# Optimization experiments

Measured on AMD Instinct MI355X. Metric: run time of the kernel, lower is better.

Reference implementation:

```python
import jax, jax.numpy as jnp
import numpy as np

NUM_ITERS = 10
G_KSIZE, G_SIGMA = 5, 0.5
BIL_KSIZE, BIL_SIG_COLOR, BIL_SIG_SPACE = 5, 0.5, 5.0
EDGE_KSIZE, EDGE_SIG_COLOR, EDGE_SIG_SPACE = 5, 0.5, 5.0


def _gauss1d(ksize, sigma):
    x = jnp.arange(ksize, dtype=jnp.float32) - ksize // 2  # odd ksize -> centered (kornia)
    g = jnp.exp(-(x * x) / (2.0 * sigma * sigma))
    return g / g.sum()


def gaussian_blur(q, ksize, sigma):
    # separable gaussian blur with reflect padding, kornia GaussianBlur2d semantics
    k = _gauss1d(ksize, sigma)
    r = ksize // 2
    B, C, H, W = q.shape
    qp = jnp.pad(q, ((0, 0), (0, 0), (r, r), (0, 0)), mode='reflect')
    q = sum(k[i] * qp[:, :, i:i + H, :] for i in range(ksize))
    qp = jnp.pad(q, ((0, 0), (0, 0), (0, 0), (r, r)), mode='reflect')
    q = sum(k[i] * qp[:, :, :, i:i + W] for i in range(ksize))
    return q


def bilateral_weights(guide, ksize, sigma_color, sigma_space):
    # kornia joint_bilateral_blur weights (l1 color distance, reflect border).
    # guide: [B, Cg, H, W] -> weights [B, K*K, H, W]; guidance is constant across
    # CRF iterations so we precompute the kernel once.
    B, Cg, H, W = guide.shape
    r = ksize // 2
    g1 = _gauss1d(ksize, sigma_space)
    space = jnp.outer(g1, g1)  # normalized 2d gaussian (kornia get_gaussian_kernel2d)
    gp = jnp.pad(guide, ((0, 0), (0, 0), (r, r), (r, r)), mode='reflect')
    inv2sc2 = -0.5 / (sigma_color * sigma_color)
    ws = []
    for dy in range(ksize):
        for dx in range(ksize):
            d = jnp.abs(gp[:, :, dy:dy + H, dx:dx + W] - guide).sum(axis=1)  # [B,H,W]
            ws.append(space[dy, dx] * jnp.exp(inv2sc2 * d * d))
    return jnp.stack(ws, axis=1)  # [B, K*K, H, W]


def bilateral_apply(q, weights, ksize):
    # q: [B,C,H,W], weights: [B,K*K,H,W]
    B, C, H, W = q.shape
    r = ksize // 2
    qp = jnp.pad(q, ((0, 0), (0, 0), (r, r), (r, r)), mode='reflect')
    num = jnp.zeros_like(q)
    idx = 0
    for dy in range(ksize):
        for dx in range(ksize):
            num = num + weights[:, idx][:, None] * qp[:, :, dy:dy + H, dx:dx + W]
            idx += 1
    den = weights.sum(axis=1)[:, None]  # [B,1,H,W]
    return num / den


def _compat(f):
    # compat matrix is -1 off-diagonal, 0 on diagonal:
    # pairwise[c] = -sum_{c'!=c} f[c'] = f[c] - sum_{c'} f[c']
    return f - f.sum(axis=1, keepdims=True)


def setup_inputs() -> dict:
    key = jax.random.key(0)
    k1, k2, k3 = jax.random.split(key, 3)
    B, C, H, W = 2, 21, 512, 512
    unary_logits = jax.random.normal(k1, (B, C, H, W), dtype=jnp.float32)
    image = jax.random.uniform(k2, (B, 3, H, W), dtype=jnp.float32)
    edges = jax.random.uniform(k3, (B, H, W), dtype=jnp.float32)
    return {"unary_logits": unary_logits, "image": image, "edges": edges}


def reference(unary_logits, image, edges):
    edges4 = edges[:, None]  # [B,1,H,W]
    w_rgb = bilateral_weights(image, BIL_KSIZE, BIL_SIG_COLOR, BIL_SIG_SPACE)
    w_edge = bilateral_weights(edges4, EDGE_KSIZE, EDGE_SIG_COLOR, EDGE_SIG_SPACE)
    q = jax.nn.softmax(unary_logits, axis=1)
    for _ in range(NUM_ITERS):
        sf = gaussian_blur(q, G_KSIZE, G_SIGMA)
        rf = bilateral_apply(q, w_rgb, BIL_KSIZE)
        ef = bilateral_apply(q, w_edge, EDGE_KSIZE)
        pairwise = _compat(sf) + _compat(rf) + _compat(ef)
        q = jax.nn.softmax(unary_logits - pairwise, axis=1)
    return q
```

## Files before the change

### kernel.cpp

```cpp
#include <hip/hip_runtime.h>
#include <math.h>

#define BATCH 2
#define NCH 21
#define CPAD 24
#define HH 512
#define WW 512
#define KS 5
#define RAD 2
#define NTAPS 25
#define NUM_ITERS 10

#define TXW 32
#define TYW 8
#define HXW (TXW + 2*RAD)
#define HYW (TYW + 2*RAD)
#define HPXW (HXW * HYW)

#define TW 32
#define TH 16
#define NTHR 512
#define SX 40
#define SY 24
#define SPX (SX * SY)
#define SCHUNK (SPX * 3)
#define EX 36
#define EY 20
#define EPX (EX * EY)
#define RING (EPX - TW*TH)

typedef _Float16 f16;
typedef _Float16 half8 __attribute__((ext_vector_type(8)));
typedef _Float16 half2v __attribute__((ext_vector_type(2)));

__device__ __forceinline__ int refl(int i, int n) {
    if (i < 0) i = -i;
    if (i >= n) i = 2*n - 2 - i;
    return i;
}

#define WSEL(h0, h1, h2, hl, t) \
    ((t) < 8 ? (h0)[(t)] : (t) < 16 ? (h1)[(t) - 8] : (t) < 24 ? (h2)[(t) - 16] : (hl))

__global__ __launch_bounds__(256) void weights_kernel(const float* __restrict__ image,
                                                      const float* __restrict__ edges,
                                                      f16* __restrict__ wcA,
                                                      f16* __restrict__ wcB16) {
    __shared__ float sr_[HYW][HXW];
    __shared__ float sg_[HYW][HXW];
    __shared__ float sb_[HYW][HXW];
    __shared__ float se_[HYW][HXW];

    const int tx = threadIdx.x;
    const int ty = threadIdx.y;
    const int tid = ty * TXW + tx;
    const int x0 = blockIdx.x * TXW;
    const int y0 = blockIdx.y * TYW;
    const int b = blockIdx.z;
    const int x = x0 + tx;
    const int y = y0 + ty;
    const size_t plane = (size_t)HH * WW;
    const float* img = image + (size_t)b * 3 * plane;
    const float* edg = edges + (size_t)b * plane;

    for (int i = tid; i < HPXW; i += TXW * TYW) {
        int ly = i / HXW, lx = i - ly * HXW;
        int gy = refl(y0 + ly - RAD, HH);
        int gx = refl(x0 + lx - RAD, WW);
        int g = gy * WW + gx;
        sr_[ly][lx] = img[g];
        sg_[ly][lx] = img[plane + g];
        sb_[ly][lx] = img[2 * plane + g];
        se_[ly][lx] = edg[g];
    }
    __syncthreads();

    float gs[3];
    gs[0] = 1.0f; gs[1] = __expf(-1.0f / 50.0f); gs[2] = __expf(-4.0f / 50.0f);
    float gb[3];
    gb[0] = 1.0f; gb[1] = __expf(-2.0f); gb[2] = __expf(-8.0f);
    float gbs = gb[0] + 2.0f * (gb[1] + gb[2]);
    gb[0] /= gbs; gb[1] /= gbs; gb[2] /= gbs;

    const float r0 = sr_[ty + RAD][tx + RAD];
    const float g0 = sg_[ty + RAD][tx + RAD];
    const float b0 = sb_[ty + RAD][tx + RAD];
    const float e0 = se_[ty + RAD][tx + RAD];

    float wr[NTAPS], we[NTAPS];
    float sr = 0.f, se = 0.f;
#pragma unroll
    for (int dy = 0; dy < KS; dy++) {
#pragma unroll
        for (int dx = 0; dx < KS; dx++) {
            float sp = gs[abs(dy - RAD)] * gs[abs(dx - RAD)];
            float d = fabsf(sr_[ty + dy][tx + dx] - r0)
                    + fabsf(sg_[ty + dy][tx + dx] - g0)
                    + fabsf(sb_[ty + dy][tx + dx] - b0);
            float w1 = sp * __expf(-2.0f * d * d);
            float de = fabsf(se_[ty + dy][tx + dx] - e0);
            float w2 = sp * __expf(-2.0f * de * de);
            wr[dy * KS + dx] = w1;
            we[dy * KS + dx] = w2;
            sr += w1;
            se += w2;
        }
    }
    float isr = 1.0f / sr, ise = 1.0f / se;
    float wt[NTAPS];
#pragma unroll
    for (int t = 0; t < NTAPS; t++) {
        int dy = t / KS, dx = t % KS;
        float g2 = gb[abs(dy - RAD)] * gb[abs(dx - RAD)];
        wt[t] = g2 + wr[t] * isr + we[t] * ise;
    }
    const size_t pixoff = (size_t)b * plane + (size_t)y * WW + x;
    half8* wo = (half8*)(wcA + pixoff * 24);
#pragma unroll
    for (int g = 0; g < 3; g++) {
        half8 v;
#pragma unroll
        for (int k = 0; k < 8; k++) v[k] = (f16)wt[g * 8 + k];
        wo[g] = v;
    }
    wcB16[pixoff] = (f16)wt[24];
}

__global__ void init_kernel(const float* __restrict__ unary,
                            f16* __restrict__ q,
                            f16* __restrict__ u16) {
    int idx = blockIdx.x * blockDim.x + threadIdx.x;
    if (idx >= BATCH * HH * WW) return;
    int p = idx % (HH * WW);
    int b = idx / (HH * WW);
    const size_t plane = (size_t)HH * WW;
    const float* u = unary + (size_t)b * NCH * plane + p;
    float l[CPAD];
    float m = -1e30f;
#pragma unroll
    for (int c = 0; c < NCH; c++) { l[c] = u[c * plane]; m = fmaxf(m, l[c]); }
    l[21] = 0.f; l[22] = 0.f; l[23] = 0.f;

    half8* uo = (half8*)(u16 + ((size_t)b * plane + p) * CPAD);
#pragma unroll
    for (int g = 0; g < 3; g++) {
        half8 v;
#pragma unroll
        for (int k = 0; k < 8; k++) v[k] = (f16)l[g * 8 + k];
        uo[g] = v;
    }

    float s = 0.f;
    float e[CPAD];
#pragma unroll
    for (int c = 0; c < NCH; c++) { e[c] = __expf(l[c] - m); s += e[c]; }
    float is = 1.0f / s;
    e[21] = 0.f; e[22] = 0.f; e[23] = 0.f;
    half8* qo = (half8*)(q + ((size_t)b * plane + p) * CPAD);
#pragma unroll
    for (int g = 0; g < 3; g++) {
        half8 v;
#pragma unroll
        for (int k = 0; k < 8; k++) v[k] = (f16)(e[g * 8 + k] * is);
        qo[g] = v;
    }
}

#define CONV_ACC_PK(acc2, lds, row0, col0, stride, W0, W1, W2, WL)                     \
    {                                                                                  \
        _Pragma("unroll")                                                              \
        for (int dy = 0; dy < KS; dy++) {                                              \
            _Pragma("unroll")                                                          \
            for (int dx = 0; dx < KS; dx++) {                                          \
                const f16 wt_ = WSEL(W0, W1, W2, WL, dy * KS + dx);                    \
                const half2v wv_ = {wt_, wt_};                                         \
                const f16* tp = (lds) + ((size_t)((row0) + dy) * (stride) + (col0) + dx) * CPAD; \
                half8 v0 = *(const half8*)(tp);                                        \
                half8 v1 = *(const half8*)(tp + 8);                                    \
                half8 v2 = *(const half8*)(tp + 16);                                   \
                acc2[0]  = __builtin_elementwise_fma(wv_, __builtin_shufflevector(v0, v0, 0, 1), acc2[0]);  \
                acc2[1]  = __builtin_elementwise_fma(wv_, __builtin_shufflevector(v0, v0, 2, 3), acc2[1]);  \
                acc2[2]  = __builtin_elementwise_fma(wv_, __builtin_shufflevector(v0, v0, 4, 5), acc2[2]);  \
                acc2[3]  = __builtin_elementwise_fma(wv_, __builtin_shufflevector(v0, v0, 6, 7), acc2[3]);  \
                acc2[4]  = __builtin_elementwise_fma(wv_, __builtin_shufflevector(v1, v1, 0, 1), acc2[4]);  \
                acc2[5]  = __builtin_elementwise_fma(wv_, __builtin_shufflevector(v1, v1, 2, 3), acc2[5]);  \
                acc2[6]  = __builtin_elementwise_fma(wv_, __builtin_shufflevector(v1, v1, 4, 5), acc2[6]);  \
                acc2[7]  = __builtin_elementwise_fma(wv_, __builtin_shufflevector(v1, v1, 6, 7), acc2[7]);  \
                acc2[8]  = __builtin_elementwise_fma(wv_, __builtin_shufflevector(v2, v2, 0, 1), acc2[8]);  \
                acc2[9]  = __builtin_elementwise_fma(wv_, __builtin_shufflevector(v2, v2, 2, 3), acc2[9]);  \
                acc2[10] = __builtin_elementwise_fma(wv_, __builtin_shufflevector(v2, v2, 4, 5), acc2[10]); \
            }                                                                          \
        }                                                                              \
    }

#define LOGITS_FROM_PK(l, acc2, U0, U1, U2)                                            \
    {                                                                                  \
        _Pragma("unroll")                                                              \
        for (int j = 0; j < 10; j++) {                                                 \
            l[2 * j]     = -(float)acc2[j][0];                                         \
            l[2 * j + 1] = -(float)acc2[j][1];                                         \
        }                                                                              \
        l[20] = -(float)acc2[10][0];                                                   \
        _Pragma("unroll")                                                              \
        for (int k = 0; k < 8; k++) l[k] += (float)U0[k];                              \
        _Pragma("unroll")                                                              \
        for (int k = 0; k < 8; k++) l[8 + k] += (float)U1[k];                          \
        _Pragma("unroll")                                                              \
        for (int k = 0; k < 5; k++) l[16 + k] += (float)U2[k];                         \
    }

template <bool FINAL>
__global__ __launch_bounds__(NTHR, 4) void crf_pair_kernel(const f16* __restrict__ qin,
                                                           const f16* __restrict__ u16,
                                                           const f16* __restrict__ wcA,
                                                           const f16* __restrict__ wcB16,
                                                           void* __restrict__ qout) {
    __shared__ __align__(16) f16 buf[SPX][CPAD];

    const int tid = threadIdx.x;
    const int ix = tid & (TW - 1);
    const int iy = tid >> 5;

    const int flat = blockIdx.x;
    const int band = flat & 7;
    const int within = flat >> 3;
    const int b = within >> 6;
    const int r = within & 63;
    const int x0 = (r & 15) * TW;
    const int y0 = (band * 4 + (r >> 4)) * TH;
    const int gx = x0 + ix;
    const int gy = y0 + iy;
    const size_t plane = (size_t)HH * WW;

    const f16* qbase = qin + (size_t)b * plane * CPAD;
    f16* lbase = &buf[0][0];
    for (int idx = tid; idx < SCHUNK; idx += NTHR) {
        int px = idx / 3, h4 = idx - px * 3;
        int sly = px / SX, slx = px - sly * SX;
        int qy = refl(y0 - 4 + sly, HH);
        int qx = refl(x0 - 4 + slx, WW);
        const f16* g = qbase + ((size_t)(qy * WW + qx)) * CPAD + h4 * 8;
        __builtin_amdgcn_global_load_lds(
            (const __attribute__((address_space(1))) void*)g,
            (__attribute__((address_space(3))) void*)(lbase + (size_t)idx * 8),
            16, 0, 0);
    }

    const size_t pixoff = (size_t)b * plane + (size_t)gy * WW + gx;
    const half8* wp = (const half8*)(wcA + pixoff * 24);
    half8 wa0 = wp[0], wa1 = wp[1], wa2 = wp[2];
    f16 wl = wcB16[pixoff];
    const half8* up = (const half8*)(u16 + pixoff * CPAD);
    half8 ui0 = up[0], ui1 = up[1], ui2 = up[2];

    const bool has_ring = tid < RING;
    int rly = 0, rlx = 0;
    half8 wr0 = {}, wr1 = {}, wr2 = {}, ur0 = {}, ur1 = {}, ur2 = {};
    f16 wrl = (f16)0.f;
    if (has_ring) {
        int t = tid;
        if (t < 72)       { rly = t / 36;       rlx = t % 36; }
        else if (t < 144) { t -= 72;  rly = 18 + t / 36; rlx = t % 36; }
        else              { t -= 144; rly = 2 + (t >> 2); int c = t & 3; rlx = (c < 2) ? c : (c + 32); }
        int rgy = y0 + rly - 2, rgx = x0 + rlx - 2;
        int cy = min(max(rgy, 0), HH - 1);
        int cx = min(max(rgx, 0), WW - 1);
        size_t rpo = (size_t)b * plane + (size_t)cy * WW + cx;
        const half8* wpr = (const half8*)(wcA + rpo * 24);
        wr0 = wpr[0]; wr1 = wpr[1]; wr2 = wpr[2];
        wrl = wcB16[rpo];
        const half8* upr = (const half8*)(u16 + rpo * CPAD);
        ur0 = upr[0]; ur1 = upr[1]; ur2 = upr[2];
    }

    __syncthreads();

    half8 qr0, qr1, qr2;
    if (has_ring) {
        half2v acc2[11];
#pragma unroll
        for (int j = 0; j < 11; j++) acc2[j] = (half2v){(f16)0.f, (f16)0.f};
        CONV_ACC_PK(acc2, lbase, rly, rlx, SX, wr0, wr1, wr2, wrl);
        float l[NCH];
        LOGITS_FROM_PK(l, acc2, ur0, ur1, ur2);
        float m = l[0];
#pragma unroll
        for (int c = 1; c < NCH; c++) m = fmaxf(m, l[c]);
        float s = 0.f;
#pragma unroll
        for (int c = 0; c < NCH; c++) { l[c] = __expf(l[c] - m); s += l[c]; }
        float is = 1.0f / s;
#pragma unroll
        for (int k = 0; k < 8; k++) qr0[k] = (f16)(l[k] * is);
#pragma unroll
        for (int k = 0; k < 8; k++) qr1[k] = (f16)(l[8 + k] * is);
#pragma unroll
        for (int k = 0; k < 5; k++) qr2[k] = (f16)(l[16 + k] * is);
        qr2[5] = (f16)0.f; qr2[6] = (f16)0.f; qr2[7] = (f16)0.f;
    }

    half8 qi0, qi1, qi2;
    {
        half2v acc2[11];
#pragma unroll
        for (int j = 0; j < 11; j++) acc2[j] = (half2v){(f16)0.f, (f16)0.f};
        CONV_ACC_PK(acc2, lbase, iy + 2, ix + 2, SX, wa0, wa1, wa2, wl);
        float l[NCH];
        LOGITS_FROM_PK(l, acc2, ui0, ui1, ui2);
        float m = l[0];
#pragma unroll
        for (int c = 1; c < NCH; c++) m = fmaxf(m, l[c]);
        float s = 0.f;
#pragma unroll
        for (int c = 0; c < NCH; c++) { l[c] = __expf(l[c] - m); s += l[c]; }
        float is = 1.0f / s;
#pragma unroll
        for (int k = 0; k < 8; k++) qi0[k] = (f16)(l[k] * is);
#pragma unroll
        for (int k = 0; k < 8; k++) qi1[k] = (f16)(l[8 + k] * is);
#pragma unroll
        for (int k = 0; k < 5; k++) qi2[k] = (f16)(l[16 + k] * is);
        qi2[5] = (f16)0.f; qi2[6] = (f16)0.f; qi2[7] = (f16)0.f;
    }

    __syncthreads();

    {
        half8* d = (half8*)(lbase + ((size_t)(iy + 2) * EX + (ix + 2)) * CPAD);
        d[0] = qi0; d[1] = qi1; d[2] = qi2;
        if (has_ring) {
            half8* dr = (half8*)(lbase + ((size_t)rly * EX + rlx) * CPAD);
            dr[0] = qr0; dr[1] = qr1; dr[2] = qr2;
        }
    }

    __syncthreads();

    {
        int ry[KS], rx[KS];
#pragma unroll
        for (int d = 0; d < KS; d++) {
            ry[d] = refl(gy + d - 2, HH) - (y0 - 2);
            rx[d] = refl(gx + d - 2, WW) - (x0 - 2);
        }
        half2v acc2[11];
#pragma unroll
        for (int j = 0; j < 11; j++) acc2[j] = (half2v){(f16)0.f, (f16)0.f};
#pragma unroll
        for (int dy = 0; dy < KS; dy++) {
#pragma unroll
            for (int dx = 0; dx < KS; dx++) {
                const f16 wt_ = WSEL(wa0, wa1, wa2, wl, dy * KS + dx);
                const half2v wv_ = {wt_, wt_};
                const f16* tp = lbase + ((size_t)ry[dy] * EX + rx[dx]) * CPAD;
                half8 v0 = *(const half8*)(tp);
                half8 v1 = *(const half8*)(tp + 8);
                half8 v2 = *(const half8*)(tp + 16);
                acc2[0]  = __builtin_elementwise_fma(wv_, __builtin_shufflevector(v0, v0, 0, 1), acc2[0]);
                acc2[1]  = __builtin_elementwise_fma(wv_, __builtin_shufflevector(v0, v0, 2, 3), acc2[1]);
                acc2[2]  = __builtin_elementwise_fma(wv_, __builtin_shufflevector(v0, v0, 4, 5), acc2[2]);
                acc2[3]  = __builtin_elementwise_fma(wv_, __builtin_shufflevector(v0, v0, 6, 7), acc2[3]);
                acc2[4]  = __builtin_elementwise_fma(wv_, __builtin_shufflevector(v1, v1, 0, 1), acc2[4]);
                acc2[5]  = __builtin_elementwise_fma(wv_, __builtin_shufflevector(v1, v1, 2, 3), acc2[5]);
                acc2[6]  = __builtin_elementwise_fma(wv_, __builtin_shufflevector(v1, v1, 4, 5), acc2[6]);
                acc2[7]  = __builtin_elementwise_fma(wv_, __builtin_shufflevector(v1, v1, 6, 7), acc2[7]);
                acc2[8]  = __builtin_elementwise_fma(wv_, __builtin_shufflevector(v2, v2, 0, 1), acc2[8]);
                acc2[9]  = __builtin_elementwise_fma(wv_, __builtin_shufflevector(v2, v2, 2, 3), acc2[9]);
                acc2[10] = __builtin_elementwise_fma(wv_, __builtin_shufflevector(v2, v2, 4, 5), acc2[10]);
            }
        }
        float l[NCH];
        LOGITS_FROM_PK(l, acc2, ui0, ui1, ui2);
        float m = l[0];
#pragma unroll
        for (int c = 1; c < NCH; c++) m = fmaxf(m, l[c]);
        float s = 0.f;
#pragma unroll
        for (int c = 0; c < NCH; c++) { l[c] = __expf(l[c] - m); s += l[c]; }
        float is = 1.0f / s;

        if (FINAL) {
            float* qo = (float*)qout + (size_t)b * NCH * plane + (size_t)gy * WW + gx;
#pragma unroll
            for (int c = 0; c < NCH; c++) qo[c * plane] = l[c] * is;
        } else {
            half8* qo = (half8*)((f16*)qout + pixoff * CPAD);
            half8 o0, o1, o2;
#pragma unroll
            for (int k = 0; k < 8; k++) o0[k] = (f16)(l[k] * is);
#pragma unroll
            for (int k = 0; k < 8; k++) o1[k] = (f16)(l[8 + k] * is);
#pragma unroll
            for (int k = 0; k < 5; k++) o2[k] = (f16)(l[16 + k] * is);
            o2[5] = (f16)0.f; o2[6] = (f16)0.f; o2[7] = (f16)0.f;
            qo[0] = o0; qo[1] = o1; qo[2] = o2;
        }
    }
}

extern "C" void kernel_launch(void* const* d_in, const int* in_sizes, int n_in,
                              void* d_out, int out_size, void* d_ws, size_t ws_size,
                              hipStream_t stream) {
    const float* unary = (const float*)d_in[0];
    const float* image = (const float*)d_in[1];
    const float* edges = (const float*)d_in[2];
    float* out = (float*)d_out;

    const size_t plane = (size_t)HH * WW;
    char* ws = (char*)d_ws;
    f16* wcA = (f16*)ws;
    char* p1 = ws + sizeof(f16) * BATCH * plane * 24;
    f16* wcB16 = (f16*)p1;
    char* p2 = p1 + sizeof(f16) * BATCH * plane;
    f16* u16 = (f16*)p2;
    char* p3 = p2 + sizeof(f16) * BATCH * plane * CPAD;
    f16* qA = (f16*)p3;
    f16* qB = qA + (size_t)BATCH * plane * CPAD;

    const int npix = BATCH * HH * WW;
    dim3 gridW(WW / TXW, HH / TYW, BATCH);
    dim3 blockW(TXW, TYW, 1);
    weights_kernel<<<gridW, blockW, 0, stream>>>(image, edges, wcA, wcB16);
    init_kernel<<<(npix + 255) / 256, 256, 0, stream>>>(unary, qA, u16);

    const int nblk = (WW / TW) * (HH / TH) * BATCH;
    f16* qa = qA;
    f16* qb = qB;
    const int npairs = NUM_ITERS / 2;
    for (int it = 0; it < npairs - 1; it++) {
        crf_pair_kernel<false><<<nblk, NTHR, 0, stream>>>(qa, u16, wcA, wcB16, (void*)qb);
        f16* t = qa; qa = qb; qb = t;
    }
    crf_pair_kernel<true><<<nblk, NTHR, 0, stream>>>(qa, u16, wcA, wcB16, (void*)out);
}
```

Before: 287.4 us.

## Compute two vertically adjacent pixels per thread to share LDS loads

Halves the thread count per block and has each thread compute two vertically adjacent output pixels. The thread walks 6 staged rows and feeds each loaded LDS neighbour into both pixels' accumulators, which cuts LDS reads per pixel. The ring (halo) work is remapped so each ring thread also handles two rows. The cost is roughly double the accumulator and weight registers per thread, which may lower occupancy (launch bounds now 256 threads, 3 blocks).

```diff
diff --git a/kernel.cpp b/kernel.cpp
--- a/kernel.cpp
+++ b/kernel.cpp
@@ -19,7 +19,7 @@
 
 #define TW 32
 #define TH 16
-#define NTHR 512
+#define NTHRP 256
 #define SX 40
 #define SY 24
 #define SPX (SX * SY)
@@ -27,7 +27,7 @@
 #define EX 36
 #define EY 20
 #define EPX (EX * EY)
-#define RING (EPX - TW*TH)
+#define RINGP 104
 
 typedef _Float16 f16;
 typedef _Float16 half8 __attribute__((ext_vector_type(8)));
@@ -166,31 +166,68 @@
     }
 }
 
-#define CONV_ACC_PK(acc2, lds, row0, col0, stride, W0, W1, W2, WL)                     \
-    {                                                                                  \
-        _Pragma("unroll")                                                              \
-        for (int dy = 0; dy < KS; dy++) {                                              \
-            _Pragma("unroll")                                                          \
-            for (int dx = 0; dx < KS; dx++) {                                          \
-                const f16 wt_ = WSEL(W0, W1, W2, WL, dy * KS + dx);                    \
-                const half2v wv_ = {wt_, wt_};                                         \
-                const f16* tp = (lds) + ((size_t)((row0) + dy) * (stride) + (col0) + dx) * CPAD; \
-                half8 v0 = *(const half8*)(tp);                                        \
-                half8 v1 = *(const half8*)(tp + 8);                                    \
-                half8 v2 = *(const half8*)(tp + 16);                                   \
-                acc2[0]  = __builtin_elementwise_fma(wv_, __builtin_shufflevector(v0, v0, 0, 1), acc2[0]);  \
-                acc2[1]  = __builtin_elementwise_fma(wv_, __builtin_shufflevector(v0, v0, 2, 3), acc2[1]);  \
-                acc2[2]  = __builtin_elementwise_fma(wv_, __builtin_shufflevector(v0, v0, 4, 5), acc2[2]);  \
-                acc2[3]  = __builtin_elementwise_fma(wv_, __builtin_shufflevector(v0, v0, 6, 7), acc2[3]);  \
-                acc2[4]  = __builtin_elementwise_fma(wv_, __builtin_shufflevector(v1, v1, 0, 1), acc2[4]);  \
-                acc2[5]  = __builtin_elementwise_fma(wv_, __builtin_shufflevector(v1, v1, 2, 3), acc2[5]);  \
-                acc2[6]  = __builtin_elementwise_fma(wv_, __builtin_shufflevector(v1, v1, 4, 5), acc2[6]);  \
-                acc2[7]  = __builtin_elementwise_fma(wv_, __builtin_shufflevector(v1, v1, 6, 7), acc2[7]);  \
-                acc2[8]  = __builtin_elementwise_fma(wv_, __builtin_shufflevector(v2, v2, 0, 1), acc2[8]);  \
-                acc2[9]  = __builtin_elementwise_fma(wv_, __builtin_shufflevector(v2, v2, 2, 3), acc2[9]);  \
-                acc2[10] = __builtin_elementwise_fma(wv_, __builtin_shufflevector(v2, v2, 4, 5), acc2[10]); \
-            }                                                                          \
-        }                                                                              \
+#define PK11(acc2, wv_, v0, v1, v2) do {                                                            \
+    acc2[0]  = __builtin_elementwise_fma(wv_, __builtin_shufflevector(v0, v0, 0, 1), acc2[0]);      \
+    acc2[1]  = __builtin_elementwise_fma(wv_, __builtin_shufflevector(v0, v0, 2, 3), acc2[1]);      \
+    acc2[2]  = __builtin_elementwise_fma(wv_, __builtin_shufflevector(v0, v0, 4, 5), acc2[2]);      \
+    acc2[3]  = __builtin_elementwise_fma(wv_, __builtin_shufflevector(v0, v0, 6, 7), acc2[3]);      \
+    acc2[4]  = __builtin_elementwise_fma(wv_, __builtin_shufflevector(v1, v1, 0, 1), acc2[4]);      \
+    acc2[5]  = __builtin_elementwise_fma(wv_, __builtin_shufflevector(v1, v1, 2, 3), acc2[5]);      \
+    acc2[6]  = __builtin_elementwise_fma(wv_, __builtin_shufflevector(v1, v1, 4, 5), acc2[6]);      \
+    acc2[7]  = __builtin_elementwise_fma(wv_, __builtin_shufflevector(v1, v1, 6, 7), acc2[7]);      \
+    acc2[8]  = __builtin_elementwise_fma(wv_, __builtin_shufflevector(v2, v2, 0, 1), acc2[8]);      \
+    acc2[9]  = __builtin_elementwise_fma(wv_, __builtin_shufflevector(v2, v2, 2, 3), acc2[9]);      \
+    acc2[10] = __builtin_elementwise_fma(wv_, __builtin_shufflevector(v2, v2, 4, 5), acc2[10]);     \
+} while (0)
+
+#define CONV_PAIR_STAGED(accA, accB, lds, row0, col0, stride,                                       \
+                         WA0, WA1, WA2, WAL, WB0, WB1, WB2, WBL)                                    \
+    {                                                                                               \
+        _Pragma("unroll")                                                                           \
+        for (int r_ = 0; r_ < 6; r_++) {                                                            \
+            _Pragma("unroll")                                                                       \
+            for (int dx_ = 0; dx_ < 5; dx_++) {                                                     \
+                const f16* tp_ = (lds) + ((size_t)((row0) + r_) * (stride) + (col0) + dx_) * CPAD;  \
+                half8 v0_ = *(const half8*)(tp_);                                                   \
+                half8 v1_ = *(const half8*)(tp_ + 8);                                               \
+                half8 v2_ = *(const half8*)(tp_ + 16);                                              \
+                if (r_ < 5) {                                                                       \
+                    const f16 wA_ = WSEL(WA0, WA1, WA2, WAL, r_ * 5 + dx_);                         \
+                    const half2v wvA_ = {wA_, wA_};                                                 \
+                    PK11(accA, wvA_, v0_, v1_, v2_);                                                \
+                }                                                                                   \
+                if (r_ >= 1) {                                                                      \
+                    const f16 wB_ = WSEL(WB0, WB1, WB2, WBL, (r_ - 1) * 5 + dx_);                   \
+                    const half2v wvB_ = {wB_, wB_};                                                 \
+                    PK11(accB, wvB_, v0_, v1_, v2_);                                                \
+                }                                                                                   \
+            }                                                                                       \
+        }                                                                                           \
+    }
+
+#define CONV_PAIR_IDX(accA, accB, lds, ryArr, rxArr, stride,                                        \
+                      WA0, WA1, WA2, WAL, WB0, WB1, WB2, WBL)                                       \
+    {                                                                                               \
+        _Pragma("unroll")                                                                           \
+        for (int r_ = 0; r_ < 6; r_++) {                                                            \
+            _Pragma("unroll")                                                                       \
+            for (int dx_ = 0; dx_ < 5; dx_++) {                                                     \
+                const f16* tp_ = (lds) + ((size_t)(ryArr)[r_] * (stride) + (rxArr)[dx_]) * CPAD;    \
+                half8 v0_ = *(const half8*)(tp_);                                                   \
+                half8 v1_ = *(const half8*)(tp_ + 8);                                               \
+                half8 v2_ = *(const half8*)(tp_ + 16);                                              \
+                if (r_ < 5) {                                                                       \
+                    const f16 wA_ = WSEL(WA0, WA1, WA2, WAL, r_ * 5 + dx_);                         \
+                    const half2v wvA_ = {wA_, wA_};                                                 \
+                    PK11(accA, wvA_, v0_, v1_, v2_);                                                \
+                }                                                                                   \
+                if (r_ >= 1) {                                                                      \
+                    const f16 wB_ = WSEL(WB0, WB1, WB2, WBL, (r_ - 1) * 5 + dx_);                   \
+                    const half2v wvB_ = {wB_, wB_};                                                 \
+                    PK11(accB, wvB_, v0_, v1_, v2_);                                                \
+                }                                                                                   \
+            }                                                                                       \
+        }                                                                                           \
     }
 
 #define LOGITS_FROM_PK(l, acc2, U0, U1, U2)                                            \
@@ -209,17 +246,54 @@
         for (int k = 0; k < 5; k++) l[16 + k] += (float)U2[k];                         \
     }
 
+__device__ __forceinline__ void finish_px(const half2v* acc2,
+                                          half8 U0, half8 U1, half8 U2,
+                                          half8& o0, half8& o1, half8& o2) {
+    float l[NCH];
+    LOGITS_FROM_PK(l, acc2, U0, U1, U2);
+    float m = l[0];
+#pragma unroll
+    for (int c = 1; c < NCH; c++) m = fmaxf(m, l[c]);
+    float s = 0.f;
+#pragma unroll
+    for (int c = 0; c < NCH; c++) { l[c] = __expf(l[c] - m); s += l[c]; }
+    float is = 1.0f / s;
+#pragma unroll
+    for (int k = 0; k < 8; k++) o0[k] = (f16)(l[k] * is);
+#pragma unroll
+    for (int k = 0; k < 8; k++) o1[k] = (f16)(l[8 + k] * is);
+#pragma unroll
+    for (int k = 0; k < 5; k++) o2[k] = (f16)(l[16 + k] * is);
+    o2[5] = (f16)0.f; o2[6] = (f16)0.f; o2[7] = (f16)0.f;
+}
+
+__device__ __forceinline__ void finish_px_f32(const half2v* acc2,
+                                              half8 U0, half8 U1, half8 U2,
+                                              float* qo, size_t plane) {
+    float l[NCH];
+    LOGITS_FROM_PK(l, acc2, U0, U1, U2);
+    float m = l[0];
+#pragma unroll
+    for (int c = 1; c < NCH; c++) m = fmaxf(m, l[c]);
+    float s = 0.f;
+#pragma unroll
+    for (int c = 0; c < NCH; c++) { l[c] = __expf(l[c] - m); s += l[c]; }
+    float is = 1.0f / s;
+#pragma unroll
+    for (int c = 0; c < NCH; c++) qo[c * plane] = l[c] * is;
+}
+
 template <bool FINAL>
-__global__ __launch_bounds__(NTHR, 4) void crf_pair_kernel(const f16* __restrict__ qin,
-                                                           const f16* __restrict__ u16,
-                                                           const f16* __restrict__ wcA,
-                                                           const f16* __restrict__ wcB16,
-                                                           void* __restrict__ qout) {
+__global__ __launch_bounds__(NTHRP, 3) void crf_pair_kernel(const f16* __restrict__ qin,
+                                                            const f16* __restrict__ u16,
+                                                            const f16* __restrict__ wcA,
+                                                            const f16* __restrict__ wcB16,
+                                                            void* __restrict__ qout) {
     __shared__ __align__(16) f16 buf[SPX][CPAD];
 
     const int tid = threadIdx.x;
     const int ix = tid & (TW - 1);
-    const int iy = tid >> 5;
+    const int iyp = tid >> 5;
 
     const int flat = blockIdx.x;
     const int band = flat & 7;
@@ -229,12 +303,12 @@
     const int x0 = (r & 15) * TW;
     const int y0 = (band * 4 + (r >> 4)) * TH;
     const int gx = x0 + ix;
-    const int gy = y0 + iy;
+    const int gy0 = y0 + 2 * iyp;
     const size_t plane = (size_t)HH * WW;
 
     const f16* qbase = qin + (size_t)b * plane * CPAD;
     f16* lbase = &buf[0][0];
-    for (int idx = tid; idx < SCHUNK; idx += NTHR) {
+    for (int idx = tid; idx < SCHUNK; idx += NTHRP) {
         int px = idx / 3, h4 = idx - px * 3;
         int sly = px / SX, slx = px - sly * SX;
         int qy = refl(y0 - 4 + sly, HH);
@@ -246,154 +320,119 @@
             16, 0, 0);
     }
 
-    const size_t pixoff = (size_t)b * plane + (size_t)gy * WW + gx;
-    const half8* wp = (const half8*)(wcA + pixoff * 24);
-    half8 wa0 = wp[0], wa1 = wp[1], wa2 = wp[2];
-    f16 wl = wcB16[pixoff];
-    const half8* up = (const half8*)(u16 + pixoff * CPAD);
-    half8 ui0 = up[0], ui1 = up[1], ui2 = up[2];
-
-    const bool has_ring = tid < RING;
-    int rly = 0, rlx = 0;
-    half8 wr0 = {}, wr1 = {}, wr2 = {}, ur0 = {}, ur1 = {}, ur2 = {};
-    f16 wrl = (f16)0.f;
+    const size_t pix0 = (size_t)b * plane + (size_t)gy0 * WW + gx;
+    const size_t pix1 = pix0 + WW;
+    const half8* wpa = (const half8*)(wcA + pix0 * 24);
+    half8 wa0 = wpa[0], wa1 = wpa[1], wa2 = wpa[2];
+    f16 wal = wcB16[pix0];
+    const half8* wpb = (const half8*)(wcA + pix1 * 24);
+    half8 wb0 = wpb[0], wb1 = wpb[1], wb2 = wpb[2];
+    f16 wbl = wcB16[pix1];
+    const half8* upa = (const half8*)(u16 + pix0 * CPAD);
+    half8 ua0 = upa[0], ua1 = upa[1], ua2 = upa[2];
+    const half8* upb = (const half8*)(u16 + pix1 * CPAD);
+    half8 ub0 = upb[0], ub1 = upb[1], ub2 = upb[2];
+
+    const bool has_ring = tid < RINGP;
+    int rlx = 0, rly = 0;
+    half8 wr0a = {}, wr1a = {}, wr2a = {}, wr0b = {}, wr1b = {}, wr2b = {};
+    f16 wrla = (f16)0.f, wrlb = (f16)0.f;
+    half8 ur0a = {}, ur1a = {}, ur2a = {}, ur0b = {}, ur1b = {}, ur2b = {};
     if (has_ring) {
         int t = tid;
-        if (t < 72)       { rly = t / 36;       rlx = t % 36; }
-        else if (t < 144) { t -= 72;  rly = 18 + t / 36; rlx = t % 36; }
-        else              { t -= 144; rly = 2 + (t >> 2); int c = t & 3; rlx = (c < 2) ? c : (c + 32); }
-        int rgy = y0 + rly - 2, rgx = x0 + rlx - 2;
-        int cy = min(max(rgy, 0), HH - 1);
-        int cx = min(max(rgx, 0), WW - 1);
-        size_t rpo = (size_t)b * plane + (size_t)cy * WW + cx;
-        const half8* wpr = (const half8*)(wcA + rpo * 24);
-        wr0 = wpr[0]; wr1 = wpr[1]; wr2 = wpr[2];
-        wrl = wcB16[rpo];
-        const half8* upr = (const half8*)(u16 + rpo * CPAD);
-        ur0 = upr[0]; ur1 = upr[1]; ur2 = upr[2];
+        if (t < 36)      { rlx = t;      rly = 0;  }
+        else if (t < 72) { rlx = t - 36; rly = 18; }
+        else {
+            t -= 72;
+            int side = t >> 4;
+            int u = t & 15;
+            rlx = (u & 1) + side * 34;
+            rly = 2 + (u >> 1) * 2;
+        }
+        int rgx = x0 + rlx - 2;
+        int rgy0 = y0 + rly - 2;
+        int cx  = min(max(rgx, 0), WW - 1);
+        int cy0 = min(max(rgy0, 0), HH - 1);
+        int cy1 = min(max(rgy0 + 1, 0), HH - 1);
+        size_t rp0 = (size_t)b * plane + (size_t)cy0 * WW + cx;
+        size_t rp1 = (size_t)b * plane + (size_t)cy1 * WW + cx;
+        const half8* w0p = (const half8*)(wcA + rp0 * 24);
+        wr0a = w0p[0]; wr1a = w0p[1]; wr2a = w0p[2];
+        wrla = wcB16[rp0];
+        const half8* w1p = (const half8*)(wcA + rp1 * 24);
+        wr0b = w1p[0]; wr1b = w1p[1]; wr2b = w1p[2];
+        wrlb = wcB16[rp1];
+        const half8* u0p = (const half8*)(u16 + rp0 * CPAD);
+        ur0a = u0p[0]; ur1a = u0p[1]; ur2a = u0p[2];
+        const half8* u1p = (const half8*)(u16 + rp1 * CPAD);
+        ur0b = u1p[0]; ur1b = u1p[1]; ur2b = u1p[2];
     }
 
     __syncthreads();
 
-    half8 qr0, qr1, qr2;
+    half8 qr0a, qr1a, qr2a, qr0b, qr1b, qr2b;
     if (has_ring) {
-        half2v acc2[11];
-#pragma unroll
-        for (int j = 0; j < 11; j++) acc2[j] = (half2v){(f16)0.f, (f16)0.f};
-        CONV_ACC_PK(acc2, lbase, rly, rlx, SX, wr0, wr1, wr2, wrl);
-        float l[NCH];
-        LOGITS_FROM_PK(l, acc2, ur0, ur1, ur2);
-        float m = l[0];
-#pragma unroll
-        for (int c = 1; c < NCH; c++) m = fmaxf(m, l[c]);
-        float s = 0.f;
-#pragma unroll
-        for (int c = 0; c < NCH; c++) { l[c] = __expf(l[c] - m); s += l[c]; }
-        float is = 1.0f / s;
-#pragma unroll
-        for (int k = 0; k < 8; k++) qr0[k] = (f16)(l[k] * is);
-#pragma unroll
-        for (int k = 0; k < 8; k++) qr1[k] = (f16)(l[8 + k] * is);
-#pragma unroll
-        for (int k = 0; k < 5; k++) qr2[k] = (f16)(l[16 + k] * is);
-        qr2[5] = (f16)0.f; qr2[6] = (f16)0.f; qr2[7] = (f16)0.f;
-    }
-
-    half8 qi0, qi1, qi2;
+        half2v accA[11], accB[11];
+#pragma unroll
+        for (int j = 0; j < 11; j++) { accA[j] = (half2v){(f16)0.f, (f16)0.f}; accB[j] = accA[j]; }
+        CONV_PAIR_STAGED(accA, accB, lbase, rly, rlx, SX,
+                         wr0a, wr1a, wr2a, wrla, wr0b, wr1b, wr2b, wrlb);
+        finish_px(accA, ur0a, ur1a, ur2a, qr0a, qr1a, qr2a);
+        finish_px(accB, ur0b, ur1b, ur2b, qr0b, qr1b, qr2b);
+    }
+
+    half8 qi0a, qi1a, qi2a, qi0b, qi1b, qi2b;
     {
-        half2v acc2[11];
-#pragma unroll
-        for (int j = 0; j < 11; j++) acc2[j] = (half2v){(f16)0.f, (f16)0.f};
-        CONV_ACC_PK(acc2, lbase, iy + 2, ix + 2, SX, wa0, wa1, wa2, wl);
-        float l[NCH];
-        LOGITS_FROM_PK(l, acc2, ui0, ui1, ui2);
-        float m = l[0];
-#pragma unroll
-        for (int c = 1; c < NCH; c++) m = fmaxf(m, l[c]);
-        float s = 0.f;
-#pragma unroll
-        for (int c = 0; c < NCH; c++) { l[c] = __expf(l[c] - m); s += l[c]; }
-        float is = 1.0f / s;
-#pragma unroll
-        for (int k = 0; k < 8; k++) qi0[k] = (f16)(l[k] * is);
-#pragma unroll
-        for (int k = 0; k < 8; k++) qi1[k] = (f16)(l[8 + k] * is);
-#pragma unroll
-        for (int k = 0; k < 5; k++) qi2[k] = (f16)(l[16 + k] * is);
-        qi2[5] = (f16)0.f; qi2[6] = (f16)0.f; qi2[7] = (f16)0.f;
+        half2v accA[11], accB[11];
+#pragma unroll
+        for (int j = 0; j < 11; j++) { accA[j] = (half2v){(f16)0.f, (f16)0.f}; accB[j] = accA[j]; }
+        CONV_PAIR_STAGED(accA, accB, lbase, 2 * iyp + 2, ix + 2, SX,
+                         wa0, wa1, wa2, wal, wb0, wb1, wb2, wbl);
+        finish_px(accA, ua0, ua1, ua2, qi0a, qi1a, qi2a);
+        finish_px(accB, ub0, ub1, ub2, qi0b, qi1b, qi2b);
     }
 
     __syncthreads();
 
     {
-        half8* d = (half8*)(lbase + ((size_t)(iy + 2) * EX + (ix + 2)) * CPAD);
-        d[0] = qi0; d[1] = qi1; d[2] = qi2;
+        half8* d0 = (half8*)(lbase + ((size_t)(2 * iyp + 2) * EX + (ix + 2)) * CPAD);
+        d0[0] = qi0a; d0[1] = qi1a; d0[2] = qi2a;
+        half8* d1 = (half8*)(lbase + ((size_t)(2 * iyp + 3) * EX + (ix + 2)) * CPAD);
+        d1[0] = qi0b; d1[1] = qi1b; d1[2] = qi2b;
         if (has_ring) {
-            half8* dr = (half8*)(lbase + ((size_t)rly * EX + rlx) * CPAD);
-            dr[0] = qr0; dr[1] = qr1; dr[2] = qr2;
+            half8* e0 = (half8*)(lbase + ((size_t)rly * EX + rlx) * CPAD);
+            e0[0] = qr0a; e0[1] = qr1a; e0[2] = qr2a;
+            half8* e1 = (half8*)(lbase + ((size_t)(rly + 1) * EX + rlx) * CPAD);
+            e1[0] = qr0b; e1[1] = qr1b; e1[2] = qr2b;
         }
     }
 
     __syncthreads();
 
     {
-        int ry[KS], rx[KS];
-#pragma unroll
-        for (int d = 0; d < KS; d++) {
-            ry[d] = refl(gy + d - 2, HH) - (y0 - 2);
-            rx[d] = refl(gx + d - 2, WW) - (x0 - 2);
-        }
-        half2v acc2[11];
-#pragma unroll
-        for (int j = 0; j < 11; j++) acc2[j] = (half2v){(f16)0.f, (f16)0.f};
-#pragma unroll
-        for (int dy = 0; dy < KS; dy++) {
-#pragma unroll
-            for (int dx = 0; dx < KS; dx++) {
-                const f16 wt_ = WSEL(wa0, wa1, wa2, wl, dy * KS + dx);
-                const half2v wv_ = {wt_, wt_};
-                const f16* tp = lbase + ((size_t)ry[dy] * EX + rx[dx]) * CPAD;
-                half8 v0 = *(const half8*)(tp);
-                half8 v1 = *(const half8*)(tp + 8);
-                half8 v2 = *(const half8*)(tp + 16);
-                acc2[0]  = __builtin_elementwise_fma(wv_, __builtin_shufflevector(v0, v0, 0, 1), acc2[0]);
-                acc2[1]  = __builtin_elementwise_fma(wv_, __builtin_shufflevector(v0, v0, 2, 3), acc2[1]);
-                acc2[2]  = __builtin_elementwise_fma(wv_, __builtin_shufflevector(v0, v0, 4, 5), acc2[2]);
-                acc2[3]  = __builtin_elementwise_fma(wv_, __builtin_shufflevector(v0, v0, 6, 7), acc2[3]);
-                acc2[4]  = __builtin_elementwise_fma(wv_, __builtin_shufflevector(v1, v1, 0, 1), acc2[4]);
-                acc2[5]  = __builtin_elementwise_fma(wv_, __builtin_shufflevector(v1, v1, 2, 3), acc2[5]);
-                acc2[6]  = __builtin_elementwise_fma(wv_, __builtin_shufflevector(v1, v1, 4, 5), acc2[6]);
-                acc2[7]  = __builtin_elementwise_fma(wv_, __builtin_shufflevector(v1, v1, 6, 7), acc2[7]);
-                acc2[8]  = __builtin_elementwise_fma(wv_, __builtin_shufflevector(v2, v2, 0, 1), acc2[8]);
-                acc2[9]  = __builtin_elementwise_fma(wv_, __builtin_shufflevector(v2, v2, 2, 3), acc2[9]);
-                acc2[10] = __builtin_elementwise_fma(wv_, __builtin_shufflevector(v2, v2, 4, 5), acc2[10]);
-            }
-        }
-        float l[NCH];
-        LOGITS_FROM_PK(l, acc2, ui0, ui1, ui2);
-        float m = l[0];
-#pragma unroll
-        for (int c = 1; c < NCH; c++) m = fmaxf(m, l[c]);
-        float s = 0.f;
-#pragma unroll
-        for (int c = 0; c < NCH; c++) { l[c] = __expf(l[c] - m); s += l[c]; }
-        float is = 1.0f / s;
+        int ry_[6], rx_[5];
+#pragma unroll
+        for (int d = 0; d < 6; d++) ry_[d] = refl(gy0 + d - 2, HH) - (y0 - 2);
+#pragma unroll
+        for (int d = 0; d < 5; d++) rx_[d] = refl(gx + d - 2, WW) - (x0 - 2);
+        half2v accA[11], accB[11];
+#pragma unroll
+        for (int j = 0; j < 11; j++) { accA[j] = (half2v){(f16)0.f, (f16)0.f}; accB[j] = accA[j]; }
+        CONV_PAIR_IDX(accA, accB, lbase, ry_, rx_, EX,
+                      wa0, wa1, wa2, wal, wb0, wb1, wb2, wbl);
 
         if (FINAL) {
-            float* qo = (float*)qout + (size_t)b * NCH * plane + (size_t)gy * WW + gx;
-#pragma unroll
-            for (int c = 0; c < NCH; c++) qo[c * plane] = l[c] * is;
+            float* qo0 = (float*)qout + (size_t)b * NCH * plane + (size_t)gy0 * WW + gx;
+            finish_px_f32(accA, ua0, ua1, ua2, qo0, plane);
+            finish_px_f32(accB, ub0, ub1, ub2, qo0 + WW, plane);
         } else {
-            half8* qo = (half8*)((f16*)qout + pixoff * CPAD);
             half8 o0, o1, o2;
-#pragma unroll
-            for (int k = 0; k < 8; k++) o0[k] = (f16)(l[k] * is);
-#pragma unroll
-            for (int k = 0; k < 8; k++) o1[k] = (f16)(l[8 + k] * is);
-#pragma unroll
-            for (int k = 0; k < 5; k++) o2[k] = (f16)(l[16 + k] * is);
-            o2[5] = (f16)0.f; o2[6] = (f16)0.f; o2[7] = (f16)0.f;
-            qo[0] = o0; qo[1] = o1; qo[2] = o2;
+            finish_px(accA, ua0, ua1, ua2, o0, o1, o2);
+            half8* qo0 = (half8*)((f16*)qout + pix0 * CPAD);
+            qo0[0] = o0; qo0[1] = o1; qo0[2] = o2;
+            finish_px(accB, ub0, ub1, ub2, o0, o1, o2);
+            half8* qo1 = (half8*)((f16*)qout + pix1 * CPAD);
+            qo1[0] = o0; qo1[1] = o1; qo1[2] = o2;
         }
     }
 }
@@ -428,8 +467,8 @@
     f16* qb = qB;
     const int npairs = NUM_ITERS / 2;
     for (int it = 0; it < npairs - 1; it++) {
-        crf_pair_kernel<false><<<nblk, NTHR, 0, stream>>>(qa, u16, wcA, wcB16, (void*)qb);
+        crf_pair_kernel<false><<<nblk, NTHRP, 0, stream>>>(qa, u16, wcA, wcB16, (void*)qb);
         f16* t = qa; qa = qb; qb = t;
     }
-    crf_pair_kernel<true><<<nblk, NTHR, 0, stream>>>(qa, u16, wcA, wcB16, (void*)out);
-}
+    crf_pair_kernel<true><<<nblk, NTHRP, 0, stream>>>(qa, u16, wcA, wcB16, (void*)out);
+}
```

After: 496.4 us. 1.73x slower.
